# Performance work log

Measured on AMD Instinct MI355X. Metric: run time of the kernel, lower is better.

## Reference

```python
import jax, jax.numpy as jnp
import numpy as np

N2, N1, N0 = 16000, 4000, 1000   # leaf / mid / target node counts
DEG = 32                          # sampled neighbors per target
IN_DIM, OUT_DIM, H = 256, 64, 4
NEG = -9e15
ALPHA = 0.2                       # LeakyReLU slope


def setup_inputs() -> dict:
    key = jax.random.key(0)
    ks = jax.random.split(key, 10)
    s = 0.05  # xavier-ish scale
    x = jax.random.normal(ks[0], (N2, IN_DIM), jnp.float32)
    W0 = jax.random.normal(ks[1], (H, IN_DIM, OUT_DIM), jnp.float32) * s
    a0 = jax.random.normal(ks[2], (H, 2 * OUT_DIM), jnp.float32) * s
    W1 = jax.random.normal(ks[3], (H, OUT_DIM * H, OUT_DIM), jnp.float32) * s
    a1 = jax.random.normal(ks[4], (H, 2 * OUT_DIM), jnp.float32) * s
    lin_W = jax.random.normal(ks[5], (OUT_DIM * H, OUT_DIM * H), jnp.float32) * s
    lin_b = jax.random.normal(ks[6], (OUT_DIM * H,), jnp.float32) * s
    # level-1 edges: n1 targets, each with DEG sampled leaf neighbors + self-loop
    adj1_tgt = jnp.concatenate([jnp.repeat(jnp.arange(N1), DEG), jnp.arange(N1)]).astype(jnp.int32)
    adj1_nbr = jnp.concatenate([jax.random.randint(ks[7], (N1 * DEG,), 0, N2),
                                jnp.arange(N1)]).astype(jnp.int32)
    # level-0 edges: n0 targets, each with DEG sampled mid neighbors + self-loop
    adj0_tgt = jnp.concatenate([jnp.repeat(jnp.arange(N0), DEG), jnp.arange(N0)]).astype(jnp.int32)
    adj0_nbr = jnp.concatenate([jax.random.randint(ks[8], (N0 * DEG,), 0, N1),
                                jnp.arange(N0)]).astype(jnp.int32)
    return {"x": x, "W0": W0, "a0": a0, "W1": W1, "a1": a1,
            "lin_W": lin_W, "lin_b": lin_b,
            "adj1_tgt": adj1_tgt, "adj1_nbr": adj1_nbr,
            "adj0_tgt": adj0_tgt, "adj0_nbr": adj0_nbr,
            "n0": N0, "n1": N1}


def _att_layer(x, W, a, tgt, nbr, T):
    # x: [N, D], W: [H, D, O], a: [H, 2O]; multi-head GAT layer (eval mode, no dropout)
    h = jnp.einsum('nd,hdo->hno', x, W)                      # [H, N, O]
    O = h.shape[-1]
    e = jax.nn.leaky_relu(
        jnp.einsum('heo,ho->he', h[:, tgt], a[:, :O]) +
        jnp.einsum('heo,ho->he', h[:, nbr], a[:, O:]), ALPHA)  # [H, E]
    N = h.shape[1]
    att = jnp.full((h.shape[0], T, N), NEG, x.dtype).at[:, tgt, nbr].set(e)
    att = jax.nn.softmax(att, axis=-1)                        # dense edge-softmax
    hp = jax.nn.elu(jnp.einsum('htn,hno->hto', att, h))       # [H, T, O]
    return jnp.transpose(hp, (1, 0, 2)).reshape(T, -1)        # cat heads -> [T, H*O]


def reference(x, W0, a0, W1, a1, lin_W, lin_b,
              adj1_tgt, adj1_nbr, adj0_tgt, adj0_nbr, n0, n1):
    x1 = _att_layer(x, W0, a0, adj1_tgt, adj1_nbr, n1)   # [n1, H*O]
    x2 = _att_layer(x1, W1, a1, adj0_tgt, adj0_nbr, n0)  # [n0, H*O]
    return jnp.tanh(x2 @ lin_W.T + lin_b)                # Linear + Tanh
```

## Files before the change

kernel.cpp:

```cpp
#include <hip/hip_runtime.h>
#include <math.h>

#define N2C 16000
#define N1C 4000
#define N0C 1000
#define DEG 32
#define NHEAD 4
#define ALPHA 0.2f
#define LDP 264

typedef __attribute__((ext_vector_type(8))) short bf16x8;
typedef __attribute__((ext_vector_type(4))) float f32x4;

__device__ __forceinline__ ushort f2bf(float f) {
    unsigned u = __float_as_uint(f);
    unsigned r = (u + 0x7fffu + ((u >> 16) & 1u)) >> 16;
    return (ushort)r;
}
__device__ __forceinline__ float bf2f(ushort h) {
    return __uint_as_float(((unsigned)h) << 16);
}

__global__ __launch_bounds__(256) void repack_kernel(
    const float* __restrict__ W0, const float* __restrict__ W1,
    const float* __restrict__ linW,
    ushort* __restrict__ Wth, ushort* __restrict__ Wtl)
{
    int g = blockIdx.x * 256 + threadIdx.x;
    int mat = g >> 16;
    int idx = g & 65535;
    int c = idx >> 8, k = idx & 255;
    float v;
    if (mat == 0)      v = W0[(c >> 6) * (256 * 64) + k * 64 + (c & 63)];
    else if (mat == 1) v = W1[(c >> 6) * (256 * 64) + k * 64 + (c & 63)];
    else               v = linW[c * 256 + k];
    ushort h = f2bf(v);
    __builtin_nontemporal_store(h, &Wth[g]);
    __builtin_nontemporal_store(f2bf(v - bf2f(h)), &Wtl[g]);
}

__global__ __launch_bounds__(256) void gemm1_kernel(
    const float* __restrict__ Af,
    const ushort* __restrict__ Bh, const ushort* __restrict__ Bl,
    const float* __restrict__ avec,
    float* __restrict__ out, float* __restrict__ s_t, float* __restrict__ s_n)
{
    __shared__ ushort sah[32 * LDP];
    __shared__ ushort sal[32 * LDP];
    const int wave = threadIdx.x >> 6, lane = threadIdx.x & 63;
    const int quad = lane >> 4, l16 = lane & 15;
    const int row0 = blockIdx.x * 32;
    const int col0 = wave * 64;

    for (int idx = threadIdx.x; idx < 32 * 64; idx += 256) {
        int row = idx >> 6, c4 = idx & 63;
        float4 f = ((const float4*)Af)[(size_t)(row0 + row) * 64 + c4];
        ushort4 h, l;
        h.x = f2bf(f.x); l.x = f2bf(f.x - bf2f(h.x));
        h.y = f2bf(f.y); l.y = f2bf(f.y - bf2f(h.y));
        h.z = f2bf(f.z); l.z = f2bf(f.z - bf2f(h.z));
        h.w = f2bf(f.w); l.w = f2bf(f.w - bf2f(h.w));
        *(ushort4*)(&sah[row * LDP + c4 * 4]) = h;
        *(ushort4*)(&sal[row * LDP + c4 * 4]) = l;
    }
    __syncthreads();

    f32x4 acc[2][4];
#pragma unroll
    for (int r = 0; r < 2; ++r)
#pragma unroll
        for (int c = 0; c < 4; ++c) acc[r][c] = (f32x4){0.f, 0.f, 0.f, 0.f};
    const int kbase = quad * 8;

    for (int k0 = 0; k0 < 256; k0 += 32) {
        bf16x8 a_h[2], a_l[2], b_h[4], b_l[4];
#pragma unroll
        for (int r = 0; r < 2; ++r) {
            int loff = (r * 16 + l16) * LDP + k0 + kbase;
            a_h[r] = *(const bf16x8*)(&sah[loff]);
            a_l[r] = *(const bf16x8*)(&sal[loff]);
        }
#pragma unroll
        for (int c = 0; c < 4; ++c) {
            int off = (col0 + c * 16 + l16) * 256 + k0 + kbase;
            b_h[c] = *(const bf16x8*)(Bh + off);
            b_l[c] = *(const bf16x8*)(Bl + off);
        }
#pragma unroll
        for (int r = 0; r < 2; ++r)
#pragma unroll
            for (int c = 0; c < 4; ++c) {
                acc[r][c] = __builtin_amdgcn_mfma_f32_16x16x32_bf16(a_h[r], b_h[c], acc[r][c], 0, 0, 0);
                acc[r][c] = __builtin_amdgcn_mfma_f32_16x16x32_bf16(a_h[r], b_l[c], acc[r][c], 0, 0, 0);
                acc[r][c] = __builtin_amdgcn_mfma_f32_16x16x32_bf16(a_l[r], b_h[c], acc[r][c], 0, 0, 0);
            }
    }

#pragma unroll
    for (int r = 0; r < 2; ++r)
#pragma unroll
        for (int c = 0; c < 4; ++c) {
            int col = col0 + c * 16 + l16;
#pragma unroll
            for (int reg = 0; reg < 4; ++reg) {
                int row = row0 + r * 16 + quad * 4 + reg;
                __builtin_nontemporal_store(acc[r][c][reg], &out[(size_t)row * 256 + col]);
            }
        }

    float at[4], an[4];
#pragma unroll
    for (int c = 0; c < 4; ++c) {
        at[c] = avec[wave * 128 + c * 16 + l16];
        an[c] = avec[wave * 128 + 64 + c * 16 + l16];
    }
#pragma unroll
    for (int r = 0; r < 2; ++r) {
        float pt[4] = {0.f, 0.f, 0.f, 0.f}, pn[4] = {0.f, 0.f, 0.f, 0.f};
#pragma unroll
        for (int c = 0; c < 4; ++c)
#pragma unroll
            for (int reg = 0; reg < 4; ++reg) {
                pt[reg] += acc[r][c][reg] * at[c];
                pn[reg] += acc[r][c][reg] * an[c];
            }
#pragma unroll
        for (int reg = 0; reg < 4; ++reg)
#pragma unroll
            for (int m = 1; m < 16; m <<= 1) {
                pt[reg] += __shfl_xor(pt[reg], m);
                pn[reg] += __shfl_xor(pn[reg], m);
            }
        if (l16 == 0) {
#pragma unroll
            for (int reg = 0; reg < 4; ++reg) {
                int row = row0 + r * 16 + quad * 4 + reg;
                __builtin_nontemporal_store(pt[reg], &s_t[wave * N2C + row]);
                __builtin_nontemporal_store(pn[reg], &s_n[wave * N2C + row]);
            }
        }
    }
}

__global__ __launch_bounds__(256) void att_gemm_kernel(
    const float* __restrict__ h0, const int* __restrict__ nbr_arr,
    const float* __restrict__ s_t, const float* __restrict__ s_n,
    const ushort* __restrict__ Bh, const ushort* __restrict__ Bl,
    const float* __restrict__ avec,
    float* __restrict__ h1, float* __restrict__ st2, float* __restrict__ sn2)
{
    __shared__ ushort sah[16 * LDP];
    __shared__ ushort sal[16 * LDP];
    __shared__ int   nbr_s[16][DEG + 1];
    __shared__ float att_w[16][NHEAD][DEG + 1];

    const int wave = threadIdx.x >> 6, lane = threadIdx.x & 63;
    const int quad = lane >> 4, l16 = lane & 15;
    const int row0 = blockIdx.x * 16;

    for (int idx = threadIdx.x; idx < 16 * (DEG + 1); idx += 256) {
        int tt = idx / (DEG + 1), e = idx - tt * (DEG + 1);
        nbr_s[tt][e] = (e < DEG) ? nbr_arr[(row0 + tt) * DEG + e]
                                 : nbr_arr[N1C * DEG + row0 + tt];
    }
    __syncthreads();

    for (int i = 0; i < 4; ++i) {
        const int tl = wave * 4 + i;
        const int gt = row0 + tl;
        int me = (lane <= DEG) ? nbr_s[tl][lane] : 0;
        int k = (lane <= DEG) ? 1 : 0;
#pragma unroll
        for (int j = 0; j < DEG; ++j) {
            int v = __shfl(me, j);
            if (j < lane && v == me) k = 0;
        }
#pragma unroll
        for (int hd = 0; hd < NHEAD; ++hd) {
            float e = s_t[hd * N2C + gt] + s_n[hd * N2C + me];
            e = (e >= 0.f) ? e : ALPHA * e;
            float em = k ? e : -1e30f;
            float m = em;
#pragma unroll
            for (int off = 1; off < 64; off <<= 1) m = fmaxf(m, __shfl_xor(m, off));
            float w = k ? __expf(e - m) : 0.f;
            float Z = w;
#pragma unroll
            for (int off = 1; off < 64; off <<= 1) Z += __shfl_xor(Z, off);
            if (lane <= DEG) att_w[tl][hd][lane] = w / Z;
        }
        __syncthreads();

        const int hh = lane >> 4;
        float4 acc = make_float4(0.f, 0.f, 0.f, 0.f);
#pragma unroll
        for (int e = 0; e <= DEG; ++e) {
            float w = att_w[tl][hh][e];
            float4 v = ((const float4*)h0)[(size_t)nbr_s[tl][e] * 64 + lane];
            acc.x += w * v.x; acc.y += w * v.y;
            acc.z += w * v.z; acc.w += w * v.w;
        }
        acc.x = (acc.x > 0.f) ? acc.x : expm1f(acc.x);
        acc.y = (acc.y > 0.f) ? acc.y : expm1f(acc.y);
        acc.z = (acc.z > 0.f) ? acc.z : expm1f(acc.z);
        acc.w = (acc.w > 0.f) ? acc.w : expm1f(acc.w);
        ushort4 h4, l4;
        h4.x = f2bf(acc.x); l4.x = f2bf(acc.x - bf2f(h4.x));
        h4.y = f2bf(acc.y); l4.y = f2bf(acc.y - bf2f(h4.y));
        h4.z = f2bf(acc.z); l4.z = f2bf(acc.z - bf2f(h4.z));
        h4.w = f2bf(acc.w); l4.w = f2bf(acc.w - bf2f(h4.w));
        *(ushort4*)(&sah[tl * LDP + lane * 4]) = h4;
        *(ushort4*)(&sal[tl * LDP + lane * 4]) = l4;
    }
    __syncthreads();

    f32x4 acc2[4];
#pragma unroll
    for (int c = 0; c < 4; ++c) acc2[c] = (f32x4){0.f, 0.f, 0.f, 0.f};
    const int col0 = wave * 64;
    const int kbase = quad * 8;
    for (int k0 = 0; k0 < 256; k0 += 32) {
        bf16x8 a_h, a_l, b_h[4], b_l[4];
        int loff = l16 * LDP + k0 + kbase;
        a_h = *(const bf16x8*)(&sah[loff]);
        a_l = *(const bf16x8*)(&sal[loff]);
#pragma unroll
        for (int c = 0; c < 4; ++c) {
            int off = (col0 + c * 16 + l16) * 256 + k0 + kbase;
            b_h[c] = *(const bf16x8*)(Bh + off);
            b_l[c] = *(const bf16x8*)(Bl + off);
        }
#pragma unroll
        for (int c = 0; c < 4; ++c) {
            acc2[c] = __builtin_amdgcn_mfma_f32_16x16x32_bf16(a_h, b_h[c], acc2[c], 0, 0, 0);
            acc2[c] = __builtin_amdgcn_mfma_f32_16x16x32_bf16(a_h, b_l[c], acc2[c], 0, 0, 0);
            acc2[c] = __builtin_amdgcn_mfma_f32_16x16x32_bf16(a_l, b_h[c], acc2[c], 0, 0, 0);
        }
    }
#pragma unroll
    for (int c = 0; c < 4; ++c) {
        int col = col0 + c * 16 + l16;
#pragma unroll
        for (int reg = 0; reg < 4; ++reg) {
            int row = row0 + quad * 4 + reg;
            __builtin_nontemporal_store(acc2[c][reg], &h1[(size_t)row * 256 + col]);
        }
    }

    float at[4], an[4];
#pragma unroll
    for (int c = 0; c < 4; ++c) {
        at[c] = avec[wave * 128 + c * 16 + l16];
        an[c] = avec[wave * 128 + 64 + c * 16 + l16];
    }
    float pt[4] = {0.f, 0.f, 0.f, 0.f}, pn[4] = {0.f, 0.f, 0.f, 0.f};
#pragma unroll
    for (int c = 0; c < 4; ++c)
#pragma unroll
        for (int reg = 0; reg < 4; ++reg) {
            pt[reg] += acc2[c][reg] * at[c];
            pn[reg] += acc2[c][reg] * an[c];
        }
#pragma unroll
    for (int reg = 0; reg < 4; ++reg)
#pragma unroll
        for (int m = 1; m < 16; m <<= 1) {
            pt[reg] += __shfl_xor(pt[reg], m);
            pn[reg] += __shfl_xor(pn[reg], m);
        }
    if (l16 == 0) {
#pragma unroll
        for (int reg = 0; reg < 4; ++reg) {
            int row = row0 + quad * 4 + reg;
            __builtin_nontemporal_store(pt[reg], &st2[wave * N1C + row]);
            __builtin_nontemporal_store(pn[reg], &sn2[wave * N1C + row]);
        }
    }
}

__global__ __launch_bounds__(256) void att_lin_kernel(
    const float* __restrict__ h1, const int* __restrict__ nbr_arr,
    const float* __restrict__ s_t, const float* __restrict__ s_n,
    const ushort* __restrict__ Bh, const ushort* __restrict__ Bl,
    const float* __restrict__ bias, float* __restrict__ out)
{
    __shared__ int   nbr_s[4][DEG + 1];
    __shared__ float att_w[4][NHEAD][DEG + 1];
    __shared__ float x2[4][256];

    const int wave = threadIdx.x >> 6, lane = threadIdx.x & 63;
    const int blk = blockIdx.x;

    for (int idx = threadIdx.x; idx < 4 * (DEG + 1); idx += 256) {
        int tt = idx / (DEG + 1), e = idx - tt * (DEG + 1);
        nbr_s[tt][e] = (e < DEG) ? nbr_arr[(blk * 4 + tt) * DEG + e]
                                 : nbr_arr[N0C * DEG + blk * 4 + tt];
    }
    __syncthreads();

    {
        const int tl = wave;
        const int gt = blk * 4 + tl;
        int me = (lane <= DEG) ? nbr_s[tl][lane] : 0;
        int k = (lane <= DEG) ? 1 : 0;
#pragma unroll
        for (int j = 0; j < DEG; ++j) {
            int v = __shfl(me, j);
            if (j < lane && v == me) k = 0;
        }
#pragma unroll
        for (int hd = 0; hd < NHEAD; ++hd) {
            float e = s_t[hd * N1C + gt] + s_n[hd * N1C + me];
            e = (e >= 0.f) ? e : ALPHA * e;
            float em = k ? e : -1e30f;
            float m = em;
#pragma unroll
            for (int off = 1; off < 64; off <<= 1) m = fmaxf(m, __shfl_xor(m, off));
            float w = k ? __expf(e - m) : 0.f;
            float Z = w;
#pragma unroll
            for (int off = 1; off < 64; off <<= 1) Z += __shfl_xor(Z, off);
            if (lane <= DEG) att_w[tl][hd][lane] = w / Z;
        }
    }
    __syncthreads();
    {
        const int tl = wave;
        const int hh = lane >> 4;
        float4 acc = make_float4(0.f, 0.f, 0.f, 0.f);
#pragma unroll
        for (int e = 0; e <= DEG; ++e) {
            float w = att_w[tl][hh][e];
            float4 v = ((const float4*)h1)[(size_t)nbr_s[tl][e] * 64 + lane];
            acc.x += w * v.x; acc.y += w * v.y;
            acc.z += w * v.z; acc.w += w * v.w;
        }
        acc.x = (acc.x > 0.f) ? acc.x : expm1f(acc.x);
        acc.y = (acc.y > 0.f) ? acc.y : expm1f(acc.y);
        acc.z = (acc.z > 0.f) ? acc.z : expm1f(acc.z);
        acc.w = (acc.w > 0.f) ? acc.w : expm1f(acc.w);
        *(float4*)(&x2[tl][lane * 4]) = acc;
    }
    __syncthreads();

    const int c = threadIdx.x;
    float v0 = 0.f, v1 = 0.f, v2 = 0.f, v3 = 0.f;
    for (int k8 = 0; k8 < 32; ++k8) {
        bf16x8 hb = *(const bf16x8*)(Bh + c * 256 + k8 * 8);
        bf16x8 lb = *(const bf16x8*)(Bl + c * 256 + k8 * 8);
#pragma unroll
        for (int j = 0; j < 8; ++j) {
            float wv = bf2f((ushort)hb[j]) + bf2f((ushort)lb[j]);
            int kk = k8 * 8 + j;
            v0 += x2[0][kk] * wv; v1 += x2[1][kk] * wv;
            v2 += x2[2][kk] * wv; v3 += x2[3][kk] * wv;
        }
    }
    float b = bias[c];
    out[(size_t)(blk * 4 + 0) * 256 + c] = tanhf(v0 + b);
    out[(size_t)(blk * 4 + 1) * 256 + c] = tanhf(v1 + b);
    out[(size_t)(blk * 4 + 2) * 256 + c] = tanhf(v2 + b);
    out[(size_t)(blk * 4 + 3) * 256 + c] = tanhf(v3 + b);
}

extern "C" void kernel_launch(void* const* d_in, const int* in_sizes, int n_in,
                              void* d_out, int out_size, void* d_ws, size_t ws_size,
                              hipStream_t stream)
{
    const float* x    = (const float*)d_in[0];
    const float* W0   = (const float*)d_in[1];
    const float* a0   = (const float*)d_in[2];
    const float* W1   = (const float*)d_in[3];
    const float* a1   = (const float*)d_in[4];
    const float* linW = (const float*)d_in[5];
    const float* linb = (const float*)d_in[6];
    const int* adj1_nbr = (const int*)d_in[8];
    const int* adj0_nbr = (const int*)d_in[10];

    char* base = (char*)d_ws;
    ushort* Wth = (ushort*)base;
    ushort* Wtl = Wth + 3 * 65536;
    float*  st  = (float*)(base + 786432);
    float*  sn  = (float*)(base + 1048576);
    float*  st2 = (float*)(base + 1310720);
    float*  sn2 = (float*)(base + 1376256);
    float*  h0  = (float*)(base + 1441792);
    float*  h1  = (float*)(base + 17825792);

    repack_kernel<<<768, 256, 0, stream>>>(W0, W1, linW, Wth, Wtl);

    gemm1_kernel<<<N2C / 32, 256, 0, stream>>>(x, Wth, Wtl, a0, h0, st, sn);

    att_gemm_kernel<<<N1C / 16, 256, 0, stream>>>(
        h0, adj1_nbr, st, sn, Wth + 65536, Wtl + 65536, a1, h1, st2, sn2);

    att_lin_kernel<<<N0C / 4, 256, 0, stream>>>(
        h1, adj0_nbr, st2, sn2, Wth + 131072, Wtl + 131072, linb, (float*)d_out);
}
```

Measured before the change: 175.9 us.

## Split layer-1 attention from GEMM into per-target kernel; read linear weights as fp32

The fused attention+GEMM kernel, which ran 16 targets per block with serial per-target loops, becomes two kernels. A new attention kernel runs one block per target, with the four waves each handling one head's softmax and then splitting the neighbour gather four ways with an LDS reduction. It writes bf16 hi/lo activations to global memory, and a separate gemm2 kernel reads them back for the MFMA GEMM. The final linear layer now reads fp32 linW directly instead of repacked bf16 hi/lo pairs, so the repack kernel is smaller. The split exposes more parallelism in the gather at the cost of an extra launch and a global round-trip for the intermediate activations.

```diff
diff --git a/kernel.cpp b/kernel.cpp
--- a/kernel.cpp
+++ b/kernel.cpp
@@ -20,20 +20,21 @@
 __device__ __forceinline__ float bf2f(ushort h) {
     return __uint_as_float(((unsigned)h) << 16);
 }
+__device__ __forceinline__ unsigned long long pack4(ushort a, ushort b, ushort c, ushort d) {
+    return (unsigned long long)a | ((unsigned long long)b << 16) |
+           ((unsigned long long)c << 32) | ((unsigned long long)d << 48);
+}
 
 __global__ __launch_bounds__(256) void repack_kernel(
     const float* __restrict__ W0, const float* __restrict__ W1,
-    const float* __restrict__ linW,
     ushort* __restrict__ Wth, ushort* __restrict__ Wtl)
 {
     int g = blockIdx.x * 256 + threadIdx.x;
     int mat = g >> 16;
     int idx = g & 65535;
     int c = idx >> 8, k = idx & 255;
-    float v;
-    if (mat == 0)      v = W0[(c >> 6) * (256 * 64) + k * 64 + (c & 63)];
-    else if (mat == 1) v = W1[(c >> 6) * (256 * 64) + k * 64 + (c & 63)];
-    else               v = linW[c * 256 + k];
+    const float* W = mat ? W1 : W0;
+    float v = W[(c >> 6) * (256 * 64) + k * 64 + (c & 63)];
     ushort h = f2bf(v);
     __builtin_nontemporal_store(h, &Wth[g]);
     __builtin_nontemporal_store(f2bf(v - bf2f(h)), &Wtl[g]);
@@ -142,88 +143,104 @@
     }
 }
 
-__global__ __launch_bounds__(256) void att_gemm_kernel(
-    const float* __restrict__ h0, const int* __restrict__ nbr_arr,
+__global__ __launch_bounds__(256) void att_kernel(
+    const float* __restrict__ hprev, const int* __restrict__ nbr_arr,
     const float* __restrict__ s_t, const float* __restrict__ s_n,
+    ushort* __restrict__ outhi, ushort* __restrict__ outlo, int T, int Nsrc)
+{
+    __shared__ int nbr[DEG + 1];
+    __shared__ float att_s[NHEAD][DEG + 3];
+    __shared__ float4 red[4][64];
+    const int tgt = blockIdx.x;
+    const int t = threadIdx.x;
+    const int lane = t & 63;
+    if (t < DEG) nbr[t] = nbr_arr[tgt * DEG + t];
+    else if (t == DEG) nbr[DEG] = nbr_arr[T * DEG + tgt];
+    __syncthreads();
+
+    {
+        const int hd = t >> 6;
+        int me = (lane <= DEG) ? nbr[lane] : -1;
+        int k = (lane <= DEG) ? 1 : 0;
+#pragma unroll
+        for (int j = 0; j < DEG; ++j) {
+            int v = __shfl(me, j);
+            if (j < lane && v == me) k = 0;
+        }
+        float e = s_t[hd * Nsrc + tgt] + ((lane <= DEG) ? s_n[hd * Nsrc + me] : 0.f);
+        e = (e >= 0.f) ? e : ALPHA * e;
+        float em = k ? e : -1e30f;
+        float m = em;
+#pragma unroll
+        for (int off = 1; off < 64; off <<= 1) m = fmaxf(m, __shfl_xor(m, off));
+        float w = k ? __expf(e - m) : 0.f;
+        float Z = w;
+#pragma unroll
+        for (int off = 1; off < 64; off <<= 1) Z += __shfl_xor(Z, off);
+        if (lane <= DEG) att_s[hd][lane] = w / Z;
+    }
+    __syncthreads();
+
+    const int cq = t & 63;
+    const int rg = t >> 6;
+    const int hd = cq >> 4;
+    const float4* hp4 = (const float4*)hprev;
+    float4 acc = make_float4(0.f, 0.f, 0.f, 0.f);
+#pragma unroll
+    for (int ii = 0; ii < 9; ++ii) {
+        int i = rg + ii * 4;
+        if (i <= DEG) {
+            float w = att_s[hd][i];
+            float4 v = hp4[(size_t)nbr[i] * 64 + cq];
+            acc.x += w * v.x; acc.y += w * v.y;
+            acc.z += w * v.z; acc.w += w * v.w;
+        }
+    }
+    red[rg][cq] = acc;
+    __syncthreads();
+    if (t < 64) {
+        float4 s0 = red[0][t], s1 = red[1][t], s2 = red[2][t], s3 = red[3][t];
+        float4 s;
+        s.x = s0.x + s1.x + s2.x + s3.x;
+        s.y = s0.y + s1.y + s2.y + s3.y;
+        s.z = s0.z + s1.z + s2.z + s3.z;
+        s.w = s0.w + s1.w + s2.w + s3.w;
+        s.x = (s.x > 0.f) ? s.x : expm1f(s.x);
+        s.y = (s.y > 0.f) ? s.y : expm1f(s.y);
+        s.z = (s.z > 0.f) ? s.z : expm1f(s.z);
+        s.w = (s.w > 0.f) ? s.w : expm1f(s.w);
+        ushort hx = f2bf(s.x), hy = f2bf(s.y), hz = f2bf(s.z), hw = f2bf(s.w);
+        ushort lx = f2bf(s.x - bf2f(hx)), ly = f2bf(s.y - bf2f(hy));
+        ushort lz = f2bf(s.z - bf2f(hz)), lw = f2bf(s.w - bf2f(hw));
+        __builtin_nontemporal_store(pack4(hx, hy, hz, hw),
+            &((unsigned long long*)outhi)[tgt * 64 + t]);
+        __builtin_nontemporal_store(pack4(lx, ly, lz, lw),
+            &((unsigned long long*)outlo)[tgt * 64 + t]);
+    }
+}
+
+__global__ __launch_bounds__(256) void gemm2_kernel(
+    const ushort* __restrict__ Ah, const ushort* __restrict__ Al,
     const ushort* __restrict__ Bh, const ushort* __restrict__ Bl,
     const float* __restrict__ avec,
     float* __restrict__ h1, float* __restrict__ st2, float* __restrict__ sn2)
 {
-    __shared__ ushort sah[16 * LDP];
-    __shared__ ushort sal[16 * LDP];
-    __shared__ int   nbr_s[16][DEG + 1];
-    __shared__ float att_w[16][NHEAD][DEG + 1];
-
     const int wave = threadIdx.x >> 6, lane = threadIdx.x & 63;
     const int quad = lane >> 4, l16 = lane & 15;
     const int row0 = blockIdx.x * 16;
-
-    for (int idx = threadIdx.x; idx < 16 * (DEG + 1); idx += 256) {
-        int tt = idx / (DEG + 1), e = idx - tt * (DEG + 1);
-        nbr_s[tt][e] = (e < DEG) ? nbr_arr[(row0 + tt) * DEG + e]
-                                 : nbr_arr[N1C * DEG + row0 + tt];
-    }
-    __syncthreads();
-
-    for (int i = 0; i < 4; ++i) {
-        const int tl = wave * 4 + i;
-        const int gt = row0 + tl;
-        int me = (lane <= DEG) ? nbr_s[tl][lane] : 0;
-        int k = (lane <= DEG) ? 1 : 0;
-#pragma unroll
-        for (int j = 0; j < DEG; ++j) {
-            int v = __shfl(me, j);
-            if (j < lane && v == me) k = 0;
-        }
-#pragma unroll
-        for (int hd = 0; hd < NHEAD; ++hd) {
-            float e = s_t[hd * N2C + gt] + s_n[hd * N2C + me];
-            e = (e >= 0.f) ? e : ALPHA * e;
-            float em = k ? e : -1e30f;
-            float m = em;
-#pragma unroll
-            for (int off = 1; off < 64; off <<= 1) m = fmaxf(m, __shfl_xor(m, off));
-            float w = k ? __expf(e - m) : 0.f;
-            float Z = w;
-#pragma unroll
-            for (int off = 1; off < 64; off <<= 1) Z += __shfl_xor(Z, off);
-            if (lane <= DEG) att_w[tl][hd][lane] = w / Z;
-        }
-        __syncthreads();
-
-        const int hh = lane >> 4;
-        float4 acc = make_float4(0.f, 0.f, 0.f, 0.f);
-#pragma unroll
-        for (int e = 0; e <= DEG; ++e) {
-            float w = att_w[tl][hh][e];
-            float4 v = ((const float4*)h0)[(size_t)nbr_s[tl][e] * 64 + lane];
-            acc.x += w * v.x; acc.y += w * v.y;
-            acc.z += w * v.z; acc.w += w * v.w;
-        }
-        acc.x = (acc.x > 0.f) ? acc.x : expm1f(acc.x);
-        acc.y = (acc.y > 0.f) ? acc.y : expm1f(acc.y);
-        acc.z = (acc.z > 0.f) ? acc.z : expm1f(acc.z);
-        acc.w = (acc.w > 0.f) ? acc.w : expm1f(acc.w);
-        ushort4 h4, l4;
-        h4.x = f2bf(acc.x); l4.x = f2bf(acc.x - bf2f(h4.x));
-        h4.y = f2bf(acc.y); l4.y = f2bf(acc.y - bf2f(h4.y));
-        h4.z = f2bf(acc.z); l4.z = f2bf(acc.z - bf2f(h4.z));
-        h4.w = f2bf(acc.w); l4.w = f2bf(acc.w - bf2f(h4.w));
-        *(ushort4*)(&sah[tl * LDP + lane * 4]) = h4;
-        *(ushort4*)(&sal[tl * LDP + lane * 4]) = l4;
-    }
-    __syncthreads();
-
-    f32x4 acc2[4];
-#pragma unroll
-    for (int c = 0; c < 4; ++c) acc2[c] = (f32x4){0.f, 0.f, 0.f, 0.f};
     const int col0 = wave * 64;
     const int kbase = quad * 8;
+    const int arow = row0 + l16;
+
+    f32x4 acc2[4];
+#pragma unroll
+    for (int c = 0; c < 4; ++c) acc2[c] = (f32x4){0.f, 0.f, 0.f, 0.f};
+
     for (int k0 = 0; k0 < 256; k0 += 32) {
         bf16x8 a_h, a_l, b_h[4], b_l[4];
-        int loff = l16 * LDP + k0 + kbase;
-        a_h = *(const bf16x8*)(&sah[loff]);
-        a_l = *(const bf16x8*)(&sal[loff]);
+        int aoff = arow * 256 + k0 + kbase;
+        a_h = *(const bf16x8*)(Ah + aoff);
+        a_l = *(const bf16x8*)(Al + aoff);
 #pragma unroll
         for (int c = 0; c < 4; ++c) {
             int off = (col0 + c * 16 + l16) * 256 + k0 + kbase;
@@ -281,8 +298,8 @@
 __global__ __launch_bounds__(256) void att_lin_kernel(
     const float* __restrict__ h1, const int* __restrict__ nbr_arr,
     const float* __restrict__ s_t, const float* __restrict__ s_n,
-    const ushort* __restrict__ Bh, const ushort* __restrict__ Bl,
-    const float* __restrict__ bias, float* __restrict__ out)
+    const float* __restrict__ linW, const float* __restrict__ bias,
+    float* __restrict__ out)
 {
     __shared__ int   nbr_s[4][DEG + 1];
     __shared__ float att_w[4][NHEAD][DEG + 1];
@@ -344,17 +361,15 @@
     __syncthreads();
 
     const int c = threadIdx.x;
+    const float4* wrow = (const float4*)(linW + c * 256);
     float v0 = 0.f, v1 = 0.f, v2 = 0.f, v3 = 0.f;
-    for (int k8 = 0; k8 < 32; ++k8) {
-        bf16x8 hb = *(const bf16x8*)(Bh + c * 256 + k8 * 8);
-        bf16x8 lb = *(const bf16x8*)(Bl + c * 256 + k8 * 8);
-#pragma unroll
-        for (int j = 0; j < 8; ++j) {
-            float wv = bf2f((ushort)hb[j]) + bf2f((ushort)lb[j]);
-            int kk = k8 * 8 + j;
-            v0 += x2[0][kk] * wv; v1 += x2[1][kk] * wv;
-            v2 += x2[2][kk] * wv; v3 += x2[3][kk] * wv;
-        }
+    for (int q = 0; q < 64; ++q) {
+        float4 wv = wrow[q];
+        int kk = q * 4;
+        v0 += x2[0][kk] * wv.x + x2[0][kk+1] * wv.y + x2[0][kk+2] * wv.z + x2[0][kk+3] * wv.w;
+        v1 += x2[1][kk] * wv.x + x2[1][kk+1] * wv.y + x2[1][kk+2] * wv.z + x2[1][kk+3] * wv.w;
+        v2 += x2[2][kk] * wv.x + x2[2][kk+1] * wv.y + x2[2][kk+2] * wv.z + x2[2][kk+3] * wv.w;
+        v3 += x2[3][kk] * wv.x + x2[3][kk+1] * wv.y + x2[3][kk+2] * wv.z + x2[3][kk+3] * wv.w;
     }
     float b = bias[c];
     out[(size_t)(blk * 4 + 0) * 256 + c] = tanhf(v0 + b);
@@ -379,21 +394,25 @@
 
     char* base = (char*)d_ws;
     ushort* Wth = (ushort*)base;
-    ushort* Wtl = Wth + 3 * 65536;
-    float*  st  = (float*)(base + 786432);
-    float*  sn  = (float*)(base + 1048576);
-    float*  st2 = (float*)(base + 1310720);
-    float*  sn2 = (float*)(base + 1376256);
-    float*  h0  = (float*)(base + 1441792);
-    float*  h1  = (float*)(base + 17825792);
-
-    repack_kernel<<<768, 256, 0, stream>>>(W0, W1, linW, Wth, Wtl);
+    ushort* Wtl = (ushort*)(base + 262144);
+    float*  st  = (float*)(base + 524288);
+    float*  sn  = (float*)(base + 786432);
+    float*  st2 = (float*)(base + 1048576);
+    float*  sn2 = (float*)(base + 1114112);
+    ushort* xhi = (ushort*)(base + 1179648);
+    ushort* xlo = (ushort*)(base + 3276800);
+    float*  h0  = (float*)(base + 5373952);
+    float*  h1  = (float*)(base + 21757952);
+
+    repack_kernel<<<512, 256, 0, stream>>>(W0, W1, Wth, Wtl);
 
     gemm1_kernel<<<N2C / 32, 256, 0, stream>>>(x, Wth, Wtl, a0, h0, st, sn);
 
-    att_gemm_kernel<<<N1C / 16, 256, 0, stream>>>(
-        h0, adj1_nbr, st, sn, Wth + 65536, Wtl + 65536, a1, h1, st2, sn2);
+    att_kernel<<<N1C, 256, 0, stream>>>(h0, adj1_nbr, st, sn, xhi, xlo, N1C, N2C);
+
+    gemm2_kernel<<<N1C / 16, 256, 0, stream>>>(
+        xhi, xlo, Wth + 65536, Wtl + 65536, a1, h1, st2, sn2);
 
     att_lin_kernel<<<N0C / 4, 256, 0, stream>>>(
-        h1, adj0_nbr, st2, sn2, Wth + 131072, Wtl + 131072, linb, (float*)d_out);
-}
+        h1, adj0_nbr, st2, sn2, linW, linb, (float*)d_out);
+}
```

Measured after the change: 158.6 us (median of 2 runs). 1.11x faster.
